# Kernel optimization log

Measured on AMD Instinct MI355X. Metric: run time of the kernel, lower is better.

Reference implementation:

```python
import jax, jax.numpy as jnp
import numpy as np

N_NODES = 50000
N_EDGES = 800000
N_GRAPHS = 1024
BN_EPS = 1e-5

def _linear_params(key, fan_in, fan_out):
    k1, k2 = jax.random.split(key)
    lim = 1.0 / np.sqrt(fan_in)
    w = jax.random.uniform(k1, (fan_in, fan_out), jnp.float32, -lim, lim)
    b = jax.random.uniform(k2, (fan_out,), jnp.float32, -lim, lim)
    return w, b


def setup_inputs() -> dict:
    key = jax.random.key(0)
    ks = jax.random.split(key, 16)
    x = jax.random.normal(ks[0], (N_NODES, 114), jnp.float32)
    edge_index = jax.random.randint(ks[1], (2, N_EDGES), 0, N_NODES, jnp.int64)
    batch = jnp.sort(jax.random.randint(ks[2], (N_NODES,), 0, N_GRAPHS, jnp.int64))
    w1a, b1a = _linear_params(ks[3], 114, 198)
    w1b, b1b = _linear_params(ks[4], 198, 198)
    w2a, b2a = _linear_params(ks[5], 198, 64)
    w2b, b2b = _linear_params(ks[6], 64, 64)
    w3a, b3a = _linear_params(ks[7], 64, 32)
    w3b, b3b = _linear_params(ks[8], 32, 32)
    fw1, fb1 = _linear_params(ks[9], 32, 16)
    fw2, fb2 = _linear_params(ks[10], 16, 8)
    ow, ob = _linear_params(ks[11], 8, 2)
    g1 = jnp.ones((198,), jnp.float32); be1 = jnp.zeros((198,), jnp.float32)
    g2 = jnp.ones((64,), jnp.float32); be2 = jnp.zeros((64,), jnp.float32)
    g3 = jnp.ones((32,), jnp.float32); be3 = jnp.zeros((32,), jnp.float32)
    return dict(x=x, edge_index=edge_index, batch=batch,
                w1a=w1a, b1a=b1a, w1b=w1b, b1b=b1b, g1=g1, be1=be1,
                w2a=w2a, b2a=b2a, w2b=w2b, b2b=b2b, g2=g2, be2=be2,
                w3a=w3a, b3a=b3a, w3b=w3b, b3b=b3b, g3=g3, be3=be3,
                fw1=fw1, fb1=fb1, fw2=fw2, fb2=fb2, ow=ow, ob=ob)


def _gin_conv(x, src, dst, wa, ba, wb, bb):
    # GINConv, eps=0: h_i = MLP((1+eps)*x_i + sum_{j->i} x_j)
    agg = jax.ops.segment_sum(x[src], dst, num_segments=N_NODES)
    h = x + agg
    h = jax.nn.relu(h @ wa + ba) @ wb + bb
    return h


def _batchnorm(h, gamma, beta):
    # training-mode BN over the node axis (biased variance, as torch)
    mean = jnp.mean(h, axis=0)
    var = jnp.var(h, axis=0)
    return (h - mean) * jax.lax.rsqrt(var + BN_EPS) * gamma + beta


def reference(x, edge_index, batch,
              w1a, b1a, w1b, b1b, g1, be1,
              w2a, b2a, w2b, b2b, g2, be2,
              w3a, b3a, w3b, b3b, g3, be3,
              fw1, fb1, fw2, fb2, ow, ob):
    src, dst = edge_index[0], edge_index[1]
    h = jax.nn.relu(_gin_conv(x, src, dst, w1a, b1a, w1b, b1b))
    h = _batchnorm(h, g1, be1)
    h = jax.nn.relu(_gin_conv(h, src, dst, w2a, b2a, w2b, b2b))
    h = _batchnorm(h, g2, be2)
    h = jax.nn.relu(_gin_conv(h, src, dst, w3a, b3a, w3b, b3b))
    h = _batchnorm(h, g3, be3)
    g = jax.ops.segment_sum(h, batch, num_segments=N_GRAPHS)  # global_add_pool
    g = jax.nn.relu(g @ fw1 + fb1)
    g = jax.nn.relu(g @ fw2 + fb2)
    return g @ ow + ob
```

## Files before the change

### kernel.cpp

```cpp
#include <hip/hip_runtime.h>

#define NODES  50000
#define EDGES  800000
#define GRAPHS 1024
#define P      200

#define SCAN_BLK 256
#define SCAN_NB  ((NODES + SCAN_BLK - 1) / SCAN_BLK)

typedef __attribute__((ext_vector_type(8))) short short8v;
typedef __attribute__((ext_vector_type(4))) short short4v;
typedef __attribute__((ext_vector_type(4))) float f32x4;

__device__ __forceinline__ ushort f2bf(float f) {
    uint u = __float_as_uint(f);
    u = u + 0x7FFFu + ((u >> 16) & 1u);
    return (ushort)(u >> 16);
}

__global__ void hist_kernel(const int* __restrict__ dst, int* __restrict__ deg,
                            const int* __restrict__ batch, int* __restrict__ cnt) {
    int e = blockIdx.x * blockDim.x + threadIdx.x;
    if (e < EDGES) atomicAdd(&deg[dst[e]], 1);
    if (e < NODES) atomicAdd(&cnt[batch[e]], 1);
}

__global__ void scan_part(const int* __restrict__ deg, int* __restrict__ part) {
    __shared__ int sh[SCAN_BLK];
    int t = threadIdx.x;
    int n = blockIdx.x * SCAN_BLK + t;
    sh[t] = (n < NODES) ? deg[n] : 0;
    __syncthreads();
    for (int off = SCAN_BLK / 2; off > 0; off >>= 1) {
        if (t < off) sh[t] += sh[t + off];
        __syncthreads();
    }
    if (t == 0) part[blockIdx.x] = sh[0];
}

__global__ void scan_scan(int* __restrict__ part) {
    __shared__ int sh[SCAN_BLK];
    int t = threadIdx.x;
    int v = (t < SCAN_NB) ? part[t] : 0;
    sh[t] = v;
    __syncthreads();
    for (int off = 1; off < SCAN_BLK; off <<= 1) {
        int u = 0;
        if (t >= off) u = sh[t - off];
        __syncthreads();
        if (t >= off) sh[t] += u;
        __syncthreads();
    }
    if (t < SCAN_NB) part[t] = sh[t] - v;
}

__global__ void scan_expand(const int* __restrict__ deg, const int* __restrict__ part,
                            int* __restrict__ rowstart, int* __restrict__ cursor) {
    __shared__ int sh[SCAN_BLK];
    int t = threadIdx.x;
    int n = blockIdx.x * SCAN_BLK + t;
    int v = (n < NODES) ? deg[n] : 0;
    sh[t] = v;
    __syncthreads();
    for (int off = 1; off < SCAN_BLK; off <<= 1) {
        int u = 0;
        if (t >= off) u = sh[t - off];
        __syncthreads();
        if (t >= off) sh[t] += u;
        __syncthreads();
    }
    int excl = sh[t] - v + part[blockIdx.x];
    if (n < NODES) {
        rowstart[n] = excl;
        cursor[n]   = excl;
        if (n == NODES - 1) rowstart[NODES] = excl + v;
    }
}

__global__ void scatter_kernel(const int* __restrict__ src, const int* __restrict__ dst,
                               int* __restrict__ cursor, int* __restrict__ csrc) {
    int e = blockIdx.x * blockDim.x + threadIdx.x;
    if (e < EDGES) {
        int p = atomicAdd(&cursor[dst[e]], 1);
        csrc[p] = src[e];
    }
}

__global__ void pad_all(const float* __restrict__ w1a, const float* __restrict__ w1b,
                        const float* __restrict__ w2a, const float* __restrict__ w2b,
                        const float* __restrict__ w3a, const float* __restrict__ w3b,
                        ushort* __restrict__ WF1, ushort* __restrict__ WF2,
                        ushort* __restrict__ WF3, ushort* __restrict__ WF4,
                        ushort* __restrict__ WF5, ushort* __restrict__ WF6) {
    int s = blockIdx.x * blockDim.x + threadIdx.x;
    const float* W; ushort* out; int K, N, NCH, CT, base;
    if      (s < 65536)  { W = w1a; out = WF1; K = 114; N = 198; NCH = 4; CT = 16; base = 0; }
    else if (s < 180224) { W = w1b; out = WF2; K = 198; N = 198; NCH = 7; CT = 16; base = 65536; }
    else if (s < 208896) { W = w2a; out = WF3; K = 198; N = 64;  NCH = 7; CT = 4;  base = 180224; }
    else if (s < 217088) { W = w2b; out = WF4; K = 64;  N = 64;  NCH = 2; CT = 4;  base = 208896; }
    else if (s < 225280) { W = w3a; out = WF5; K = 64;  N = 32;  NCH = 2; CT = 4;  base = 217088; }
    else if (s < 229376) { W = w3b; out = WF6; K = 32;  N = 32;  NCH = 1; CT = 4;  base = 225280; }
    else return;
    int idx = s - base;
    int half = NCH * CT * 512;
    int h = idx / half, r = idx % half;
    int j = r & 7, col = (r >> 3) & 15, kg = (r >> 7) & 3;
    int rest = r >> 9;
    int ct = rest % CT, c = rest / CT;
    int k = c * 32 + kg * 8 + j;
    int n = ct * 16 + col;
    float v = (k < K && n < N) ? W[k * N + n] : 0.0f;
    ushort hi = f2bf(v);
    if (h == 0) out[idx] = hi;
    else {
        float hf = __uint_as_float(((uint)hi) << 16);
        out[idx] = f2bf(v - hf);
    }
}

template<int D>
__global__ void csr_agg(const float* __restrict__ feat, int fpitch,
                        const int* __restrict__ rowstart, const int* __restrict__ csrc,
                        float* __restrict__ agg, int opitch) {
    int wid  = (blockIdx.x * blockDim.x + threadIdx.x) >> 6;
    int lane = threadIdx.x & 63;
    constexpr int UNR = 8;
    if constexpr (D == 32) {
        const int half = lane >> 5, sub = lane & 31;
        const int node = 2 * wid + half;
        const bool nact = node < NODES;
        const int r0 = nact ? rowstart[node] : 0;
        const int r1 = nact ? rowstart[node + 1] : 0;
        float s = 0.0f;
        for (int base = r0; base < r1; base += 32) {
            const int myidx = (base + sub < r1) ? csrc[base + sub] : 0;
            const int cnt = min(32, r1 - base);
            int t = 0;
            for (; t + UNR <= cnt; t += UNR) {
                const float* p[UNR];
#pragma unroll
                for (int u = 0; u < UNR; u++)
                    p[u] = feat + (size_t)__shfl(myidx, 32 * half + t + u) * fpitch;
                float v[UNR];
#pragma unroll
                for (int u = 0; u < UNR; u++) v[u] = p[u][sub];
                float acc = 0.0f;
#pragma unroll
                for (int u = 0; u < UNR; u++) acc += v[u];
                s += acc;
            }
            for (; t < cnt; t++) {
                const float* fp2 = feat + (size_t)__shfl(myidx, 32 * half + t) * fpitch;
                s += fp2[sub];
            }
        }
        if (nact) agg[(size_t)node * opitch + sub] = s;
    } else if constexpr (D == 114) {
        if (wid >= NODES) return;
        const int r0 = rowstart[wid], r1 = rowstart[wid + 1];
        const bool act = lane < 57;
        float sx = 0.0f, sy = 0.0f;
        for (int base = r0; base < r1; base += 64) {
            const int myidx = (base + lane < r1) ? csrc[base + lane] : 0;
            const int cnt = min(64, r1 - base);
            int t = 0;
            for (; t + UNR <= cnt; t += UNR) {
                const float2* p[UNR];
#pragma unroll
                for (int u = 0; u < UNR; u++)
                    p[u] = (const float2*)(feat + (size_t)__shfl(myidx, t + u) * fpitch);
                float2 v[UNR];
#pragma unroll
                for (int u = 0; u < UNR; u++) if (act) v[u] = p[u][lane];
                if (act) {
                    float ax = 0.0f, ay = 0.0f;
#pragma unroll
                    for (int u = 0; u < UNR; u++) { ax += v[u].x; ay += v[u].y; }
                    sx += ax; sy += ay;
                }
            }
            for (; t < cnt; t++) {
                const float2* fp2 = (const float2*)(feat + (size_t)__shfl(myidx, t) * fpitch);
                if (act) { float2 v = fp2[lane]; sx += v.x; sy += v.y; }
            }
        }
        if (act) *(float2*)(agg + (size_t)wid * opitch + 2 * lane) = make_float2(sx, sy);
    } else {
        if (wid >= NODES) return;
        const int r0 = rowstart[wid], r1 = rowstart[wid + 1];
        float s = 0.0f;
        for (int base = r0; base < r1; base += 64) {
            const int myidx = (base + lane < r1) ? csrc[base + lane] : 0;
            const int cnt = min(64, r1 - base);
            int t = 0;
            for (; t + UNR <= cnt; t += UNR) {
                const float* p[UNR];
#pragma unroll
                for (int u = 0; u < UNR; u++)
                    p[u] = feat + (size_t)__shfl(myidx, t + u) * fpitch;
                float v[UNR];
#pragma unroll
                for (int u = 0; u < UNR; u++)
                    if (lane < D) v[u] = p[u][lane];
                if (lane < D) {
                    float acc = 0.0f;
#pragma unroll
                    for (int u = 0; u < UNR; u++) acc += v[u];
                    s += acc;
                }
            }
            for (; t < cnt; t++) {
                const float* fp2 = feat + (size_t)__shfl(myidx, t) * fpitch;
                if (lane < D) s += fp2[lane];
            }
        }
        if (lane < D) agg[(size_t)wid * opitch + lane] = s;
    }
}

__launch_bounds__(256)
__global__ void gemm_fused_l1(const float* __restrict__ X,
                              const float* __restrict__ A2,
                              const ushort* __restrict__ WF1,
                              const float* __restrict__ B1,
                              const ushort* __restrict__ WF2,
                              const float* __restrict__ B2,
                              float* __restrict__ OUT,
                              float* __restrict__ gsum, float* __restrict__ gsq) {
    constexpr int K1   = 114;
    constexpr int NCH1 = 4;
    constexpr int NCH2 = 7;
    constexpr int CT   = 16;
    constexpr int CTW  = 4;
    constexpr int NN   = 198;

    __shared__ __align__(16) ushort A_lds[2][2][2][4][16][8];
    __shared__ __align__(16) ushort M_lds[2][NCH2][2][4][16][8];
    __shared__ float shSum[256];
    __shared__ float shSq [256];

    const int tid  = threadIdx.x;
    const int lane = tid & 63;
    const int wv   = tid >> 6;
    const int node0 = blockIdx.x * 32;

    for (int n = tid; n < 256; n += 256) { shSum[n] = 0.0f; shSq[n] = 0.0f; }

    const int sr  = tid >> 3;
    const int sc4 = (tid & 7) * 4;
    const int skg = sc4 >> 3;
    const int sj0 = sc4 & 7;
    const int gn  = node0 + sr;
    const size_t fstride1 = (size_t)NCH1 * CT * 512;
    const size_t fstride2 = (size_t)NCH2 * CT * 512;

    float xv[4];
    float a2v[4];

    auto loadA = [&](int c) {
        const int k0 = c * 32 + sc4;
#pragma unroll
        for (int j = 0; j < 4; j++) {
            int gk = k0 + j;
            bool ok = (gn < NODES && gk < K1);
            xv[j]  = ok ? X[(size_t)gn * K1 + gk] : 0.0f;
            a2v[j] = ok ? A2[(size_t)gn * P + gk] : 0.0f;
        }
    };
    auto cvtStore = [&](int buf, int c) {
        const int k0 = c * 32 + sc4;
        short4v hv, lv;
#pragma unroll
        for (int j = 0; j < 4; j++) {
            int gk = k0 + j;
            float t = 0.0f;
            if (gn < NODES && gk < K1) t = xv[j] + a2v[j];
            ushort h = f2bf(t);
            float hf = __uint_as_float(((uint)h) << 16);
            ushort l = f2bf(t - hf);
            hv[j] = (short)h; lv[j] = (short)l;
        }
        *(short4v*)&A_lds[buf][0][sr >> 4][skg][sr & 15][sj0] = hv;
        *(short4v*)&A_lds[buf][1][sr >> 4][skg][sr & 15][sj0] = lv;
    };

    f32x4 acc1[2][CTW] = {};
    loadA(0);
    cvtStore(0, 0);
    __syncthreads();

    const int kg = lane >> 4, rw = lane & 15;
#pragma unroll
    for (int c = 0; c < NCH1; c++) {
        const int buf = c & 1;
        if (c + 1 < NCH1) loadA(c + 1);

        short8v ah[2], al[2];
#pragma unroll
        for (int rt = 0; rt < 2; rt++) {
            ah[rt] = *(const short8v*)&A_lds[buf][0][rt][kg][rw][0];
            al[rt] = *(const short8v*)&A_lds[buf][1][rt][kg][rw][0];
        }
        const size_t fb0 = ((size_t)(c * CT + wv * CTW)) * 512 + (size_t)lane * 8;
        short8v wh = *(const short8v*)(WF1 + fb0);
        short8v wl = *(const short8v*)(WF1 + fstride1 + fb0);
#pragma unroll
        for (int t = 0; t < CTW; t++) {
            short8v nwh, nwl;
            if (t + 1 < CTW) {
                const size_t fb = fb0 + (size_t)(t + 1) * 512;
                nwh = *(const short8v*)(WF1 + fb);
                nwl = *(const short8v*)(WF1 + fstride1 + fb);
            }
            __builtin_amdgcn_s_setprio(1);
#pragma unroll
            for (int rt = 0; rt < 2; rt++) {
                acc1[rt][t] = __builtin_amdgcn_mfma_f32_16x16x32_bf16(ah[rt], wh, acc1[rt][t], 0, 0, 0);
                acc1[rt][t] = __builtin_amdgcn_mfma_f32_16x16x32_bf16(al[rt], wh, acc1[rt][t], 0, 0, 0);
                acc1[rt][t] = __builtin_amdgcn_mfma_f32_16x16x32_bf16(ah[rt], wl, acc1[rt][t], 0, 0, 0);
            }
            __builtin_amdgcn_s_setprio(0);
            if (t + 1 < CTW) { wh = nwh; wl = nwl; }
        }
        if (c + 1 < NCH1) cvtStore((c + 1) & 1, c + 1);
        __syncthreads();
    }

    const int mg = lane >> 4, colb = lane & 15;
#pragma unroll
    for (int t = 0; t < CTW; t++) {
        const int ct = wv * CTW + t;
        if (ct >= 14) continue;
        const int n = ct * 16 + colb;
        const float bn = (n < NN) ? B1[n] : 0.0f;
        const int c2 = n >> 5, kg2 = (n >> 3) & 3, j2 = n & 7;
#pragma unroll
        for (int rt = 0; rt < 2; rt++) {
#pragma unroll
            for (int j = 0; j < 4; j++) {
                float vv = fmaxf(acc1[rt][t][j] + bn, 0.0f);
                if (n >= NN) vv = 0.0f;
                ushort h = f2bf(vv);
                float hf = __uint_as_float(((uint)h) << 16);
                ushort l = f2bf(vv - hf);
                int row = mg * 4 + j;
                M_lds[0][c2][rt][kg2][row][j2] = h;
                M_lds[1][c2][rt][kg2][row][j2] = l;
            }
        }
    }
    __syncthreads();

    f32x4 acc2[2][CTW] = {};
#pragma unroll
    for (int c = 0; c < NCH2; c++) {
        short8v ah[2], al[2];
#pragma unroll
        for (int rt = 0; rt < 2; rt++) {
            ah[rt] = *(const short8v*)&M_lds[0][c][rt][kg][rw][0];
            al[rt] = *(const short8v*)&M_lds[1][c][rt][kg][rw][0];
        }
        const size_t fb0 = ((size_t)(c * CT + wv * CTW)) * 512 + (size_t)lane * 8;
        short8v wh = *(const short8v*)(WF2 + fb0);
        short8v wl = *(const short8v*)(WF2 + fstride2 + fb0);
#pragma unroll
        for (int t = 0; t < CTW; t++) {
            short8v nwh, nwl;
            if (t + 1 < CTW) {
                const size_t fb = fb0 + (size_t)(t + 1) * 512;
                nwh = *(const short8v*)(WF2 + fb);
                nwl = *(const short8v*)(WF2 + fstride2 + fb);
            }
            __builtin_amdgcn_s_setprio(1);
#pragma unroll
            for (int rt = 0; rt < 2; rt++) {
                acc2[rt][t] = __builtin_amdgcn_mfma_f32_16x16x32_bf16(ah[rt], wh, acc2[rt][t], 0, 0, 0);
                acc2[rt][t] = __builtin_amdgcn_mfma_f32_16x16x32_bf16(al[rt], wh, acc2[rt][t], 0, 0, 0);
                acc2[rt][t] = __builtin_amdgcn_mfma_f32_16x16x32_bf16(ah[rt], wl, acc2[rt][t], 0, 0, 0);
            }
            __builtin_amdgcn_s_setprio(0);
            if (t + 1 < CTW) { wh = nwh; wl = nwl; }
        }
    }

#pragma unroll
    for (int t = 0; t < CTW; t++) {
        const int ct = wv * CTW + t;
        const int n = ct * 16 + colb;
        const float bn = (n < NN) ? B2[n] : 0.0f;
        float psum = 0.0f, psq = 0.0f;
#pragma unroll
        for (int rt = 0; rt < 2; rt++) {
#pragma unroll
            for (int j = 0; j < 4; j++) {
                int m = node0 + rt * 16 + mg * 4 + j;
                float vv = fmaxf(acc2[rt][t][j] + bn, 0.0f);
                if (m < NODES && n < NN) {
                    OUT[(size_t)m * P + n] = vv;
                    psum += vv; psq += vv * vv;
                }
            }
        }
        if (n < NN) {
            atomicAdd(&shSum[n], psum);
            atomicAdd(&shSq[n], psq);
        }
    }
    __syncthreads();
    for (int n = tid; n < NN; n += 256) {
        atomicAdd(&gsum[n], shSum[n]);
        atomicAdd(&gsq[n], shSq[n]);
    }
}

template<int K, int N, bool ADD2, bool STATS, bool BNX, bool PRE, bool ACT,
         bool WRITE, bool POOL>
__launch_bounds__(256)
__global__ void gemm_mfma(const float* __restrict__ X, int xpitch,
                          const float* __restrict__ A2, int apitch,
                          const ushort* __restrict__ WF,
                          const float* __restrict__ B,
                          const float* __restrict__ PREB,
                          const float* __restrict__ bnsum, const float* __restrict__ bnsq,
                          const float* __restrict__ gamma, const float* __restrict__ beta,
                          float* __restrict__ OUT, int opitch,
                          float* __restrict__ gsum, float* __restrict__ gsq,
                          const int* __restrict__ batch, float* __restrict__ gpool) {
    constexpr int KP  = ((K + 31) / 32) * 32;
    constexpr int NCH = KP / 32;
    constexpr int NP  = ((N + 63) / 64) * 64;
    constexpr int CT  = NP / 16;
    constexpr int CTW = CT / 4;
    static_assert(CT % 4 == 0, "col tiles must split across 4 waves");

    __shared__ __align__(16) ushort A_lds[2][2][2][4][16][8];
    __shared__ float shSum[STATS ? NP : 4];
    __shared__ float shSq [STATS ? NP : 4];
    __shared__ float shSc [BNX ? 256 : 4];
    __shared__ float shSh [BNX ? 256 : 4];

    const int tid  = threadIdx.x;
    const int lane = tid & 63;
    const int wv   = tid >> 6;
    const int node0 = blockIdx.x * 32;

    if (STATS) {
        for (int n = tid; n < NP; n += 256) { shSum[n] = 0.0f; shSq[n] = 0.0f; }
    }
    if (BNX) {
        if (tid < K) {
            float mean = bnsum[tid] * (1.0f / NODES);
            float var  = bnsq[tid] * (1.0f / NODES) - mean * mean;
            var = var < 0.0f ? 0.0f : var;
            float sc = gamma[tid] * rsqrtf(var + 1e-5f);
            shSc[tid] = sc;
            shSh[tid] = beta[tid] - mean * sc;
        }
        __syncthreads();
    }

    f32x4 acc[2][CTW] = {};

    const int sr  = tid >> 3;
    const int sc4 = (tid & 7) * 4;
    const int skg = sc4 >> 3;
    const int sj0 = sc4 & 7;
    const int gn  = node0 + sr;
    const size_t fstride = (size_t)NCH * CT * 512;

    float xvA[4], xvB[4];
    float a2vA[ADD2 ? 4 : 1], a2vB[ADD2 ? 4 : 1];

    auto loadA_A = [&](int c) {
        const int k0 = c * 32 + sc4;
#pragma unroll
        for (int j = 0; j < 4; j++) {
            int gk = k0 + j;
            bool ok = (gn < NODES && gk < K);
            xvA[j] = ok ? X[(size_t)gn * xpitch + gk] : 0.0f;
            if (ADD2) a2vA[j] = ok ? A2[(size_t)gn * apitch + gk] : 0.0f;
        }
    };
    auto loadA_B = [&](int c) {
        const int k0 = c * 32 + sc4;
#pragma unroll
        for (int j = 0; j < 4; j++) {
            int gk = k0 + j;
            bool ok = (gn < NODES && gk < K);
            xvB[j] = ok ? X[(size_t)gn * xpitch + gk] : 0.0f;
            if (ADD2) a2vB[j] = ok ? A2[(size_t)gn * apitch + gk] : 0.0f;
        }
    };
    auto cvtCore = [&](int buf, int c, const float* xv, const float* a2v) {
        const int k0 = c * 32 + sc4;
        short4v hv, lv;
#pragma unroll
        for (int j = 0; j < 4; j++) {
            int gk = k0 + j;
            float t = 0.0f;
            if (gn < NODES && gk < K) {
                t = xv[j];
                if (BNX) t = fmaf(t, shSc[gk], shSh[gk]);
                if (ADD2) t += a2v[j];
                if (PRE)  t = fmaxf(t + PREB[gk], 0.0f);
            }
            ushort h = f2bf(t);
            float hf = __uint_as_float(((uint)h) << 16);
            ushort l = f2bf(t - hf);
            hv[j] = (short)h; lv[j] = (short)l;
        }
        *(short4v*)&A_lds[buf][0][sr >> 4][skg][sr & 15][sj0] = hv;
        *(short4v*)&A_lds[buf][1][sr >> 4][skg][sr & 15][sj0] = lv;
    };

    loadA_A(0);
    if (NCH > 1) loadA_B(1);
    cvtCore(0, 0, xvA, ADD2 ? a2vA : xvA);
    __syncthreads();

    const int kg = lane >> 4, rw = lane & 15;
#pragma unroll
    for (int c = 0; c < NCH; c++) {
        const int buf = c & 1;
        if (c + 2 < NCH) {
            if ((c & 1) == 0) loadA_A(c + 2);
            else              loadA_B(c + 2);
        }

        short8v ah[2], al[2];
#pragma unroll
        for (int rt = 0; rt < 2; rt++) {
            ah[rt] = *(const short8v*)&A_lds[buf][0][rt][kg][rw][0];
            al[rt] = *(const short8v*)&A_lds[buf][1][rt][kg][rw][0];
        }

        const size_t fb0 = ((size_t)(c * CT + wv * CTW)) * 512 + (size_t)lane * 8;
        short8v wh = *(const short8v*)(WF + fb0);
        short8v wl = *(const short8v*)(WF + fstride + fb0);
#pragma unroll
        for (int t = 0; t < CTW; t++) {
            short8v nwh, nwl;
            if (t + 1 < CTW) {
                const size_t fb = fb0 + (size_t)(t + 1) * 512;
                nwh = *(const short8v*)(WF + fb);
                nwl = *(const short8v*)(WF + fstride + fb);
            }
            __builtin_amdgcn_s_setprio(1);
#pragma unroll
            for (int rt = 0; rt < 2; rt++) {
                acc[rt][t] = __builtin_amdgcn_mfma_f32_16x16x32_bf16(ah[rt], wh, acc[rt][t], 0, 0, 0);
                acc[rt][t] = __builtin_amdgcn_mfma_f32_16x16x32_bf16(al[rt], wh, acc[rt][t], 0, 0, 0);
                acc[rt][t] = __builtin_amdgcn_mfma_f32_16x16x32_bf16(ah[rt], wl, acc[rt][t], 0, 0, 0);
            }
            __builtin_amdgcn_s_setprio(0);
            if (t + 1 < CTW) { wh = nwh; wl = nwl; }
        }

        if (c + 1 < NCH) {
            if (((c + 1) & 1) == 0) cvtCore((c + 1) & 1, c + 1, xvA, ADD2 ? a2vA : xvA);
            else                    cvtCore((c + 1) & 1, c + 1, xvB, ADD2 ? a2vB : xvB);
        }
        __syncthreads();
    }

    const int mg = lane >> 4, colb = lane & 15;
#pragma unroll
    for (int t = 0; t < CTW; t++) {
        const int ct = wv * CTW + t;
        const int n = ct * 16 + colb;
        const float bn = (ACT && n < N) ? B[n] : 0.0f;
        float psum = 0.0f, psq = 0.0f;
#pragma unroll
        for (int rt = 0; rt < 2; rt++) {
#pragma unroll
            for (int j = 0; j < 4; j++) {
                int m = node0 + rt * 16 + mg * 4 + j;
                float vv = ACT ? fmaxf(acc[rt][t][j] + bn, 0.0f) : acc[rt][t][j];
                if (m < NODES && n < N) {
                    if (WRITE) OUT[(size_t)m * opitch + n] = vv;
                    if (STATS) { psum += vv; psq += vv * vv; }
                    if (POOL)  atomicAdd(&gpool[batch[m] * 32 + n], vv);
                }
            }
        }
        if (STATS && n < N) {
            atomicAdd(&shSum[n], psum);
            atomicAdd(&shSq[n], psq);
        }
    }
    if (STATS) {
        __syncthreads();
        for (int n = tid; n < N; n += 256) {
            atomicAdd(&gsum[n], shSum[n]);
            atomicAdd(&gsq[n], shSq[n]);
        }
    }
}

__global__ void head_kernel(const float* __restrict__ graw, const int* __restrict__ cnt,
                            const float* __restrict__ bnsum, const float* __restrict__ bnsq,
                            const float* __restrict__ gamma, const float* __restrict__ beta,
                            const float* __restrict__ fw1, const float* __restrict__ fb1,
                            const float* __restrict__ fw2, const float* __restrict__ fb2,
                            const float* __restrict__ ow, const float* __restrict__ ob,
                            float* __restrict__ out) {
    int gi = blockIdx.x * blockDim.x + threadIdx.x;
    if (gi >= GRAPHS) return;
    float cf = (float)cnt[gi];
    float v[32];
#pragma unroll
    for (int k = 0; k < 32; k++) {
        float mean = bnsum[k] * (1.0f / NODES);
        float var  = bnsq[k] * (1.0f / NODES) - mean * mean;
        var = var < 0.0f ? 0.0f : var;
        float sc = gamma[k] * rsqrtf(var + 1e-5f);
        float sh = beta[k] - mean * sc;
        v[k] = fmaf(graw[gi * 32 + k], sc, cf * sh);
    }
    float a1[16];
#pragma unroll
    for (int o = 0; o < 16; o++) {
        float s = fb1[o];
#pragma unroll
        for (int k = 0; k < 32; k++) s = fmaf(v[k], fw1[k * 16 + o], s);
        a1[o] = s > 0.0f ? s : 0.0f;
    }
    float a2[8];
#pragma unroll
    for (int o = 0; o < 8; o++) {
        float s = fb2[o];
#pragma unroll
        for (int k = 0; k < 16; k++) s = fmaf(a1[k], fw2[k * 8 + o], s);
        a2[o] = s > 0.0f ? s : 0.0f;
    }
#pragma unroll
    for (int o = 0; o < 2; o++) {
        float s = ob[o];
#pragma unroll
        for (int k = 0; k < 8; k++) s = fmaf(a2[k], ow[k * 2 + o], s);
        out[gi * 2 + o] = s;
    }
}

extern "C" void kernel_launch(void* const* d_in, const int* in_sizes, int n_in,
                              void* d_out, int out_size, void* d_ws, size_t ws_size,
                              hipStream_t stream) {
    const float* x     = (const float*)d_in[0];
    const int*   ei    = (const int*)d_in[1];
    const int*   batch = (const int*)d_in[2];
    const float *w1a = (const float*)d_in[3],  *b1a = (const float*)d_in[4];
    const float *w1b = (const float*)d_in[5],  *b1b = (const float*)d_in[6];
    const float *g1  = (const float*)d_in[7],  *be1 = (const float*)d_in[8];
    const float *w2a = (const float*)d_in[9],  *b2a = (const float*)d_in[10];
    const float *w2b = (const float*)d_in[11], *b2b = (const float*)d_in[12];
    const float *g2  = (const float*)d_in[13], *be2 = (const float*)d_in[14];
    const float *w3a = (const float*)d_in[15], *b3a = (const float*)d_in[16];
    const float *w3b = (const float*)d_in[17], *b3b = (const float*)d_in[18];
    const float *g3  = (const float*)d_in[19], *be3 = (const float*)d_in[20];
    const float *fw1 = (const float*)d_in[21], *fb1 = (const float*)d_in[22];
    const float *fw2 = (const float*)d_in[23], *fb2 = (const float*)d_in[24];
    const float *ow  = (const float*)d_in[25], *ob  = (const float*)d_in[26];
    const int* src = ei;
    const int* dst = ei + EDGES;

    float* ws  = (float*)d_ws;
    float* b0  = ws;
    float* b1  = ws + (size_t)NODES * P;
    float* Y2  = b1;
    float* AG2 = b1 + (size_t)NODES * 64;
    float* Y3  = b1;
    float* AG3 = b1 + (size_t)NODES * 32;

    int*   deg  = (int*)(ws + (size_t)2 * NODES * P);
    int*   cnt  = deg + NODES;
    float* SUM1 = (float*)(cnt + GRAPHS);
    float* SQ1  = SUM1 + 256;
    float* SUM2 = SQ1 + 256;
    float* SQ2  = SUM2 + 256;
    float* SUM3 = SQ2 + 256;
    float* SQ3  = SUM3 + 256;
    float* G    = SQ3 + 256;
    const size_t ZERO_ELEMS = (size_t)NODES + GRAPHS + 6 * 256 + (size_t)GRAPHS * 32;

    int* rowstart = (int*)(G + (size_t)GRAPHS * 32);
    int* cursor   = rowstart + NODES + 1;
    int* part     = cursor + NODES;
    int* csrc     = part + 256;
    uintptr_t wfp = ((uintptr_t)(csrc + EDGES) + 15) & ~(uintptr_t)15;
    ushort* WF1 = (ushort*)wfp;
    ushort* WF2 = WF1 + 65536;
    ushort* WF3 = WF2 + 114688;
    ushort* WF4 = WF3 + 28672;
    ushort* WF5 = WF4 + 8192;
    ushort* WF6 = WF5 + 8192;
    float* out = (float*)d_out;

    const int GBR  = (NODES + 31) / 32;
    const int AB   = (NODES * 64 + 255) / 256;
    const int AB2  = (((NODES + 1) / 2) * 64 + 255) / 256;
    const int EB   = (EDGES + 255) / 256;

    pad_all<<<(229376 + 255) / 256, 256, 0, stream>>>(w1a, w1b, w2a, w2b, w3a, w3b,
                                                      WF1, WF2, WF3, WF4, WF5, WF6);
    hipMemsetAsync(deg, 0, ZERO_ELEMS * sizeof(int), stream);

    hist_kernel<<<EB, 256, 0, stream>>>(dst, deg, batch, cnt);
    scan_part<<<SCAN_NB, SCAN_BLK, 0, stream>>>(deg, part);
    scan_scan<<<1, SCAN_BLK, 0, stream>>>(part);
    scan_expand<<<SCAN_NB, SCAN_BLK, 0, stream>>>(deg, part, rowstart, cursor);
    scatter_kernel<<<EB, 256, 0, stream>>>(src, dst, cursor, csrc);

    csr_agg<114><<<AB, 256, 0, stream>>>(x, 114, rowstart, csrc, b0, P);
    gemm_fused_l1<<<GBR, 256, 0, stream>>>(x, b0, WF1, b1a, WF2, b1b, b0, SUM1, SQ1);

    gemm_mfma<198, 64, false, false, true, false, false, true, false><<<GBR, 256, 0, stream>>>(
        b0, P, nullptr, 0, WF3, nullptr, nullptr, SUM1, SQ1, g1, be1,
        Y2, 64, nullptr, nullptr, nullptr, nullptr);
    csr_agg<64><<<AB, 256, 0, stream>>>(Y2, 64, rowstart, csrc, AG2, 64);
    gemm_mfma<64, 64, true, true, false, true, true, true, false><<<GBR, 256, 0, stream>>>(
        Y2, 64, AG2, 64, WF4, b2b, b2a, nullptr, nullptr, nullptr, nullptr,
        b0, 64, SUM2, SQ2, nullptr, nullptr);

    gemm_mfma<64, 32, false, false, true, false, false, true, false><<<GBR, 256, 0, stream>>>(
        b0, 64, nullptr, 0, WF5, nullptr, nullptr, SUM2, SQ2, g2, be2,
        Y3, 32, nullptr, nullptr, nullptr, nullptr);
    csr_agg<32><<<AB2, 256, 0, stream>>>(Y3, 32, rowstart, csrc, AG3, 32);
    gemm_mfma<32, 32, true, true, false, true, true, false, true><<<GBR, 256, 0, stream>>>(
        Y3, 32, AG3, 32, WF6, b3b, b3a, nullptr, nullptr, nullptr, nullptr,
        nullptr, 32, SUM3, SQ3, batch, G);

    head_kernel<<<(GRAPHS + 255) / 256, 256, 0, stream>>>(
        G, cnt, SUM3, SQ3, g3, be3, fw1, fb1, fw2, fb2, ow, ob, out);
}
```

Baseline: 413.8 us.

## Widen gemm_mfma K-chunks to 64 and prefetch two chunks ahead in fused layer-1

The generic MFMA GEMM now stages 64-wide K chunks (two 32-wide MFMA sub-steps per LDS buffer), which halves the barrier count and uses 8-element global loads and 16-byte LDS stores. Weight fragments for layers 2 and 3 are padded to an even number of 32-chunks to match. The fused layer-1 kernel switches from one-ahead to two-ahead register prefetch of its A tiles. The cost is more registers per thread and more zero-padded weight MFMAs for small K such as 32.

```diff
diff --git a/kernel.cpp b/kernel.cpp
--- a/kernel.cpp
+++ b/kernel.cpp
@@ -96,10 +96,10 @@
     const float* W; ushort* out; int K, N, NCH, CT, base;
     if      (s < 65536)  { W = w1a; out = WF1; K = 114; N = 198; NCH = 4; CT = 16; base = 0; }
     else if (s < 180224) { W = w1b; out = WF2; K = 198; N = 198; NCH = 7; CT = 16; base = 65536; }
-    else if (s < 208896) { W = w2a; out = WF3; K = 198; N = 64;  NCH = 7; CT = 4;  base = 180224; }
-    else if (s < 217088) { W = w2b; out = WF4; K = 64;  N = 64;  NCH = 2; CT = 4;  base = 208896; }
-    else if (s < 225280) { W = w3a; out = WF5; K = 64;  N = 32;  NCH = 2; CT = 4;  base = 217088; }
-    else if (s < 229376) { W = w3b; out = WF6; K = 32;  N = 32;  NCH = 1; CT = 4;  base = 225280; }
+    else if (s < 212992) { W = w2a; out = WF3; K = 198; N = 64;  NCH = 8; CT = 4;  base = 180224; }
+    else if (s < 221184) { W = w2b; out = WF4; K = 64;  N = 64;  NCH = 2; CT = 4;  base = 212992; }
+    else if (s < 229376) { W = w3a; out = WF5; K = 64;  N = 32;  NCH = 2; CT = 4;  base = 221184; }
+    else if (s < 237568) { W = w3b; out = WF6; K = 32;  N = 32;  NCH = 2; CT = 4;  base = 229376; }
     else return;
     int idx = s - base;
     int half = NCH * CT * 512;
@@ -254,20 +254,29 @@
     const size_t fstride1 = (size_t)NCH1 * CT * 512;
     const size_t fstride2 = (size_t)NCH2 * CT * 512;
 
-    float xv[4];
-    float a2v[4];
-
-    auto loadA = [&](int c) {
+    float xvA[4], a2vA[4], xvB[4], a2vB[4];
+
+    auto loadA_A = [&](int c) {
         const int k0 = c * 32 + sc4;
 #pragma unroll
         for (int j = 0; j < 4; j++) {
             int gk = k0 + j;
             bool ok = (gn < NODES && gk < K1);
-            xv[j]  = ok ? X[(size_t)gn * K1 + gk] : 0.0f;
-            a2v[j] = ok ? A2[(size_t)gn * P + gk] : 0.0f;
+            xvA[j]  = ok ? X[(size_t)gn * K1 + gk] : 0.0f;
+            a2vA[j] = ok ? A2[(size_t)gn * P + gk] : 0.0f;
         }
     };
-    auto cvtStore = [&](int buf, int c) {
+    auto loadA_B = [&](int c) {
+        const int k0 = c * 32 + sc4;
+#pragma unroll
+        for (int j = 0; j < 4; j++) {
+            int gk = k0 + j;
+            bool ok = (gn < NODES && gk < K1);
+            xvB[j]  = ok ? X[(size_t)gn * K1 + gk] : 0.0f;
+            a2vB[j] = ok ? A2[(size_t)gn * P + gk] : 0.0f;
+        }
+    };
+    auto cvtStore = [&](int buf, int c, const float* xv, const float* a2v) {
         const int k0 = c * 32 + sc4;
         short4v hv, lv;
 #pragma unroll
@@ -285,15 +294,19 @@
     };
 
     f32x4 acc1[2][CTW] = {};
-    loadA(0);
-    cvtStore(0, 0);
+    loadA_A(0);
+    loadA_B(1);
+    cvtStore(0, 0, xvA, a2vA);
     __syncthreads();
 
     const int kg = lane >> 4, rw = lane & 15;
 #pragma unroll
     for (int c = 0; c < NCH1; c++) {
         const int buf = c & 1;
-        if (c + 1 < NCH1) loadA(c + 1);
+        if (c + 2 < NCH1) {
+            if ((c & 1) == 0) loadA_A(c + 2);
+            else              loadA_B(c + 2);
+        }
 
         short8v ah[2], al[2];
 #pragma unroll
@@ -322,7 +335,10 @@
             __builtin_amdgcn_s_setprio(0);
             if (t + 1 < CTW) { wh = nwh; wl = nwl; }
         }
-        if (c + 1 < NCH1) cvtStore((c + 1) & 1, c + 1);
+        if (c + 1 < NCH1) {
+            if (((c + 1) & 1) == 0) cvtStore((c + 1) & 1, c + 1, xvA, a2vA);
+            else                    cvtStore((c + 1) & 1, c + 1, xvB, a2vB);
+        }
         __syncthreads();
     }
 
@@ -426,14 +442,16 @@
                           float* __restrict__ OUT, int opitch,
                           float* __restrict__ gsum, float* __restrict__ gsq,
                           const int* __restrict__ batch, float* __restrict__ gpool) {
-    constexpr int KP  = ((K + 31) / 32) * 32;
-    constexpr int NCH = KP / 32;
+    constexpr int NCH32 = (K + 31) / 32;
+    constexpr int CC    = (NCH32 + 1) / 2;
+    constexpr int NF    = 2 * CC;
+    constexpr int NBUF  = (CC > 1) ? 2 : 1;
     constexpr int NP  = ((N + 63) / 64) * 64;
     constexpr int CT  = NP / 16;
     constexpr int CTW = CT / 4;
     static_assert(CT % 4 == 0, "col tiles must split across 4 waves");
 
-    __shared__ __align__(16) ushort A_lds[2][2][2][4][16][8];
+    __shared__ __align__(16) ushort A_lds[NBUF][2][2][2][4][16][8];
     __shared__ float shSum[STATS ? NP : 4];
     __shared__ float shSq [STATS ? NP : 4];
     __shared__ float shSc [BNX ? 256 : 4];
@@ -462,19 +480,17 @@
     f32x4 acc[2][CTW] = {};
 
     const int sr  = tid >> 3;
-    const int sc4 = (tid & 7) * 4;
-    const int skg = sc4 >> 3;
-    const int sj0 = sc4 & 7;
+    const int so  = tid & 7;
     const int gn  = node0 + sr;
-    const size_t fstride = (size_t)NCH * CT * 512;
-
-    float xvA[4], xvB[4];
-    float a2vA[ADD2 ? 4 : 1], a2vB[ADD2 ? 4 : 1];
+    const size_t fstride = (size_t)NF * CT * 512;
+
+    float xvA[8], xvB[8];
+    float a2vA[ADD2 ? 8 : 1], a2vB[ADD2 ? 8 : 1];
 
     auto loadA_A = [&](int c) {
-        const int k0 = c * 32 + sc4;
-#pragma unroll
-        for (int j = 0; j < 4; j++) {
+        const int k0 = c * 64 + so * 8;
+#pragma unroll
+        for (int j = 0; j < 8; j++) {
             int gk = k0 + j;
             bool ok = (gn < NODES && gk < K);
             xvA[j] = ok ? X[(size_t)gn * xpitch + gk] : 0.0f;
@@ -482,9 +498,9 @@
         }
     };
     auto loadA_B = [&](int c) {
-        const int k0 = c * 32 + sc4;
-#pragma unroll
-        for (int j = 0; j < 4; j++) {
+        const int k0 = c * 64 + so * 8;
+#pragma unroll
+        for (int j = 0; j < 8; j++) {
             int gk = k0 + j;
             bool ok = (gn < NODES && gk < K);
             xvB[j] = ok ? X[(size_t)gn * xpitch + gk] : 0.0f;
@@ -492,10 +508,10 @@
         }
     };
     auto cvtCore = [&](int buf, int c, const float* xv, const float* a2v) {
-        const int k0 = c * 32 + sc4;
-        short4v hv, lv;
-#pragma unroll
-        for (int j = 0; j < 4; j++) {
+        const int k0 = c * 64 + so * 8;
+        short8v hv, lv;
+#pragma unroll
+        for (int j = 0; j < 8; j++) {
             int gk = k0 + j;
             float t = 0.0f;
             if (gn < NODES && gk < K) {
@@ -509,54 +525,57 @@
             ushort l = f2bf(t - hf);
             hv[j] = (short)h; lv[j] = (short)l;
         }
-        *(short4v*)&A_lds[buf][0][sr >> 4][skg][sr & 15][sj0] = hv;
-        *(short4v*)&A_lds[buf][1][sr >> 4][skg][sr & 15][sj0] = lv;
+        *(short8v*)&A_lds[buf][0][sr >> 4][so >> 2][so & 3][sr & 15][0] = hv;
+        *(short8v*)&A_lds[buf][1][sr >> 4][so >> 2][so & 3][sr & 15][0] = lv;
     };
 
     loadA_A(0);
-    if (NCH > 1) loadA_B(1);
+    if (CC > 1) loadA_B(1);
     cvtCore(0, 0, xvA, ADD2 ? a2vA : xvA);
     __syncthreads();
 
     const int kg = lane >> 4, rw = lane & 15;
 #pragma unroll
-    for (int c = 0; c < NCH; c++) {
-        const int buf = c & 1;
-        if (c + 2 < NCH) {
+    for (int c = 0; c < CC; c++) {
+        const int buf = (NBUF == 2) ? (c & 1) : 0;
+        if (c + 2 < CC) {
             if ((c & 1) == 0) loadA_A(c + 2);
             else              loadA_B(c + 2);
         }
 
-        short8v ah[2], al[2];
-#pragma unroll
-        for (int rt = 0; rt < 2; rt++) {
-            ah[rt] = *(const short8v*)&A_lds[buf][0][rt][kg][rw][0];
-            al[rt] = *(const short8v*)&A_lds[buf][1][rt][kg][rw][0];
-        }
-
-        const size_t fb0 = ((size_t)(c * CT + wv * CTW)) * 512 + (size_t)lane * 8;
-        short8v wh = *(const short8v*)(WF + fb0);
-        short8v wl = *(const short8v*)(WF + fstride + fb0);
-#pragma unroll
-        for (int t = 0; t < CTW; t++) {
-            short8v nwh, nwl;
-            if (t + 1 < CTW) {
-                const size_t fb = fb0 + (size_t)(t + 1) * 512;
-                nwh = *(const short8v*)(WF + fb);
-                nwl = *(const short8v*)(WF + fstride + fb);
-            }
-            __builtin_amdgcn_s_setprio(1);
+#pragma unroll
+        for (int sub = 0; sub < 2; sub++) {
+            short8v ah[2], al[2];
 #pragma unroll
             for (int rt = 0; rt < 2; rt++) {
-                acc[rt][t] = __builtin_amdgcn_mfma_f32_16x16x32_bf16(ah[rt], wh, acc[rt][t], 0, 0, 0);
-                acc[rt][t] = __builtin_amdgcn_mfma_f32_16x16x32_bf16(al[rt], wh, acc[rt][t], 0, 0, 0);
-                acc[rt][t] = __builtin_amdgcn_mfma_f32_16x16x32_bf16(ah[rt], wl, acc[rt][t], 0, 0, 0);
-            }
-            __builtin_amdgcn_s_setprio(0);
-            if (t + 1 < CTW) { wh = nwh; wl = nwl; }
-        }
-
-        if (c + 1 < NCH) {
+                ah[rt] = *(const short8v*)&A_lds[buf][0][rt][sub][kg][rw][0];
+                al[rt] = *(const short8v*)&A_lds[buf][1][rt][sub][kg][rw][0];
+            }
+            const int fc = 2 * c + sub;
+            const size_t fb0 = ((size_t)(fc * CT + wv * CTW)) * 512 + (size_t)lane * 8;
+            short8v wh = *(const short8v*)(WF + fb0);
+            short8v wl = *(const short8v*)(WF + fstride + fb0);
+#pragma unroll
+            for (int t = 0; t < CTW; t++) {
+                short8v nwh, nwl;
+                if (t + 1 < CTW) {
+                    const size_t fb = fb0 + (size_t)(t + 1) * 512;
+                    nwh = *(const short8v*)(WF + fb);
+                    nwl = *(const short8v*)(WF + fstride + fb);
+                }
+                __builtin_amdgcn_s_setprio(1);
+#pragma unroll
+                for (int rt = 0; rt < 2; rt++) {
+                    acc[rt][t] = __builtin_amdgcn_mfma_f32_16x16x32_bf16(ah[rt], wh, acc[rt][t], 0, 0, 0);
+                    acc[rt][t] = __builtin_amdgcn_mfma_f32_16x16x32_bf16(al[rt], wh, acc[rt][t], 0, 0, 0);
+                    acc[rt][t] = __builtin_amdgcn_mfma_f32_16x16x32_bf16(ah[rt], wl, acc[rt][t], 0, 0, 0);
+                }
+                __builtin_amdgcn_s_setprio(0);
+                if (t + 1 < CTW) { wh = nwh; wl = nwl; }
+            }
+        }
+
+        if (c + 1 < CC) {
             if (((c + 1) & 1) == 0) cvtCore((c + 1) & 1, c + 1, xvA, ADD2 ? a2vA : xvA);
             else                    cvtCore((c + 1) & 1, c + 1, xvB, ADD2 ? a2vB : xvB);
         }
@@ -690,7 +709,7 @@
     ushort* WF1 = (ushort*)wfp;
     ushort* WF2 = WF1 + 65536;
     ushort* WF3 = WF2 + 114688;
-    ushort* WF4 = WF3 + 28672;
+    ushort* WF4 = WF3 + 32768;
     ushort* WF5 = WF4 + 8192;
     ushort* WF6 = WF5 + 8192;
     float* out = (float*)d_out;
@@ -700,7 +719,7 @@
     const int AB2  = (((NODES + 1) / 2) * 64 + 255) / 256;
     const int EB   = (EDGES + 255) / 256;
 
-    pad_all<<<(229376 + 255) / 256, 256, 0, stream>>>(w1a, w1b, w2a, w2b, w3a, w3b,
+    pad_all<<<(237568 + 255) / 256, 256, 0, stream>>>(w1a, w1b, w2a, w2b, w3a, w3b,
                                                       WF1, WF2, WF3, WF4, WF5, WF6);
     hipMemsetAsync(deg, 0, ZERO_ELEMS * sizeof(int), stream);
 
```

After: 430.7 us. 4.1% more time.

## Prefetch A tiles two chunks ahead and pool graph sums in shared memory

Applied to the files above, without the earlier changes.

The first fused GEMM kernel now double-buffers its register prefetch of X+A2 chunks, issuing global loads two chunks ahead instead of one so load latency overlaps more MFMA work. The pooling epilogue accumulates per-graph sums in a shared-memory buffer covering up to 8 graphs per 32-node block, then flushes nonzero entries with one global atomic each. This cuts global atomic traffic to gpool. It costs extra registers for the second prefetch buffer and an added barrier, and blocks spanning more than 8 graphs fall back to global atomics.

```diff
diff --git a/kernel.cpp b/kernel.cpp
--- a/kernel.cpp
+++ b/kernel.cpp
@@ -254,20 +254,29 @@
     const size_t fstride1 = (size_t)NCH1 * CT * 512;
     const size_t fstride2 = (size_t)NCH2 * CT * 512;
 
-    float xv[4];
-    float a2v[4];
-
-    auto loadA = [&](int c) {
+    float xvA[4], a2vA[4], xvB[4], a2vB[4];
+
+    auto loadA_A = [&](int c) {
         const int k0 = c * 32 + sc4;
 #pragma unroll
         for (int j = 0; j < 4; j++) {
             int gk = k0 + j;
             bool ok = (gn < NODES && gk < K1);
-            xv[j]  = ok ? X[(size_t)gn * K1 + gk] : 0.0f;
-            a2v[j] = ok ? A2[(size_t)gn * P + gk] : 0.0f;
+            xvA[j]  = ok ? X[(size_t)gn * K1 + gk] : 0.0f;
+            a2vA[j] = ok ? A2[(size_t)gn * P + gk] : 0.0f;
         }
     };
-    auto cvtStore = [&](int buf, int c) {
+    auto loadA_B = [&](int c) {
+        const int k0 = c * 32 + sc4;
+#pragma unroll
+        for (int j = 0; j < 4; j++) {
+            int gk = k0 + j;
+            bool ok = (gn < NODES && gk < K1);
+            xvB[j]  = ok ? X[(size_t)gn * K1 + gk] : 0.0f;
+            a2vB[j] = ok ? A2[(size_t)gn * P + gk] : 0.0f;
+        }
+    };
+    auto cvtStore = [&](int buf, int c, const float* xv, const float* a2v) {
         const int k0 = c * 32 + sc4;
         short4v hv, lv;
 #pragma unroll
@@ -285,15 +294,19 @@
     };
 
     f32x4 acc1[2][CTW] = {};
-    loadA(0);
-    cvtStore(0, 0);
+    loadA_A(0);
+    loadA_B(1);
+    cvtStore(0, 0, xvA, a2vA);
     __syncthreads();
 
     const int kg = lane >> 4, rw = lane & 15;
 #pragma unroll
     for (int c = 0; c < NCH1; c++) {
         const int buf = c & 1;
-        if (c + 1 < NCH1) loadA(c + 1);
+        if (c + 2 < NCH1) {
+            if ((c & 1) == 0) loadA_A(c + 2);
+            else              loadA_B(c + 2);
+        }
 
         short8v ah[2], al[2];
 #pragma unroll
@@ -322,7 +335,10 @@
             __builtin_amdgcn_s_setprio(0);
             if (t + 1 < CTW) { wh = nwh; wl = nwl; }
         }
-        if (c + 1 < NCH1) cvtStore((c + 1) & 1, c + 1);
+        if (c + 1 < NCH1) {
+            if (((c + 1) & 1) == 0) cvtStore((c + 1) & 1, c + 1, xvA, a2vA);
+            else                    cvtStore((c + 1) & 1, c + 1, xvB, a2vB);
+        }
         __syncthreads();
     }
 
@@ -438,12 +454,20 @@
     __shared__ float shSq [STATS ? NP : 4];
     __shared__ float shSc [BNX ? 256 : 4];
     __shared__ float shSh [BNX ? 256 : 4];
+    __shared__ float shPool[POOL ? 256 : 4];
 
     const int tid  = threadIdx.x;
     const int lane = tid & 63;
     const int wv   = tid >> 6;
     const int node0 = blockIdx.x * 32;
 
+    int gfirst = 0, ng = 0;
+    if (POOL) {
+        gfirst = batch[min(node0, NODES - 1)];
+        int glast = batch[min(node0 + 31, NODES - 1)];
+        ng = glast - gfirst + 1;
+        if (tid < 256) shPool[tid] = 0.0f;
+    }
     if (STATS) {
         for (int n = tid; n < NP; n += 256) { shSum[n] = 0.0f; shSq[n] = 0.0f; }
     }
@@ -579,7 +603,11 @@
                 if (m < NODES && n < N) {
                     if (WRITE) OUT[(size_t)m * opitch + n] = vv;
                     if (STATS) { psum += vv; psq += vv * vv; }
-                    if (POOL)  atomicAdd(&gpool[batch[m] * 32 + n], vv);
+                    if (POOL) {
+                        int g = batch[m];
+                        if (ng <= 8) atomicAdd(&shPool[(g - gfirst) * 32 + n], vv);
+                        else         atomicAdd(&gpool[g * 32 + n], vv);
+                    }
                 }
             }
         }
@@ -588,12 +616,16 @@
             atomicAdd(&shSq[n], psq);
         }
     }
+    if (STATS || POOL) __syncthreads();
     if (STATS) {
-        __syncthreads();
         for (int n = tid; n < N; n += 256) {
             atomicAdd(&gsum[n], shSum[n]);
             atomicAdd(&gsq[n], shSq[n]);
         }
+    }
+    if (POOL && ng <= 8 && tid < ng * 32) {
+        float v = shPool[tid];
+        if (v != 0.0f) atomicAdd(&gpool[(gfirst + (tid >> 5)) * 32 + (tid & 31)], v);
     }
 }
 
```

Measured after the change: 404.7 us. 1.02x faster.
